# Kernel tuning notes

Measured on AMD Instinct MI355X. Metric: run time of the kernel, lower is better.

Reference implementation:

```python
import jax, jax.numpy as jnp
import numpy as np

N, K, D = 65536, 16, 64  # points, neighbors, d_out
EPS = 1e-5


def setup_inputs() -> dict:
    key = jax.random.key(0)
    ks = jax.random.split(key, 10)
    s = lambda fan: 1.0 / np.sqrt(fan)
    return {
        "p": jax.random.normal(ks[0], (N, K, 3), jnp.float32),
        "x": jax.random.normal(ks[1], (N, K, D), jnp.float32),
        # BiMLP: Conv1d(10, 2D, 1) -> BN -> ReLU -> Conv1d(2D, D, 1)
        "w1": jax.random.normal(ks[2], (10, 2 * D), jnp.float32) * s(10),
        "b1": jnp.zeros((2 * D,), jnp.float32),
        "g1": jnp.ones((2 * D,), jnp.float32),
        "be1": jnp.zeros((2 * D,), jnp.float32),
        "w2": jax.random.normal(ks[3], (2 * D, D), jnp.float32) * s(2 * D),
        "b2": jnp.zeros((D,), jnp.float32),
        # score_fn: Linear(2D, 2D, bias=False)
        "ws": jax.random.normal(ks[4], (2 * D, 2 * D), jnp.float32) * s(2 * D),
        # mlp_out: Linear(2D, D) -> BN -> ReLU
        "wo": jax.random.normal(ks[5], (2 * D, D), jnp.float32) * s(2 * D),
        "bo": jnp.zeros((D,), jnp.float32),
        "g2": jnp.ones((D,), jnp.float32),
        "be2": jnp.zeros((D,), jnp.float32),
    }


def reference(p, x, w1, b1, g1, be1, w2, b2, ws, wo, bo, g2, be2):
    # p: [N,K,3] neighbor coords (index 0 is the center), x: [N,K,D]
    center = p[:, :1, :]                                   # [N,1,3]
    diff = center - p                                      # [N,K,3]
    dist = jnp.sqrt(jnp.sum(diff * diff, axis=2, keepdims=True))  # [N,K,1]
    concat = jnp.concatenate(
        [jnp.broadcast_to(center, p.shape), p, diff, dist], axis=-1)  # [N,K,10]

    # 1x1 conv == per-point linear over channel dim
    h = jnp.einsum('nkc,cd->nkd', concat, w1) + b1          # [N,K,2D]
    # BatchNorm1d over (N,K) per channel (training-mode batch stats)
    mu = jnp.mean(h, axis=(0, 1))
    var = jnp.var(h, axis=(0, 1))
    h = (h - mu) * jax.lax.rsqrt(var + EPS) * g1 + be1
    h = jax.nn.relu(h)
    p_c = jnp.einsum('nkd,de->nke', h, w2) + b2             # [N,K,D]

    p_x = jnp.concatenate([p_c, x], axis=-1)                # [N,K,2D]
    # attention scores: linear (no bias) then softmax over neighbor dim (-2)
    scores = jax.nn.softmax(jnp.einsum('nkd,de->nke', p_x, ws), axis=-2)
    feat = jnp.sum(scores * p_x, axis=1)                    # [N,2D]

    out = feat @ wo + bo                                    # [N,D]
    mu2 = jnp.mean(out, axis=0)
    var2 = jnp.var(out, axis=0)
    out = (out - mu2) * jax.lax.rsqrt(var2 + EPS) * g2 + be2
    return jax.nn.relu(out)
```

## Files before the change

### kernel.cpp

```cpp
#include <hip/hip_runtime.h>
#include <math.h>

#define NPTS 65536
#define EPSV 1e-5f
#define B1G  256
#define B3G  1024

#define OFF_PART 0
#define OFF_S1   131072
#define OFF_S2   (OFF_S1+256)
#define OFF_PRE  (OFF_S2+128)

typedef unsigned int u32;
typedef short v8s __attribute__((ext_vector_type(8)));
typedef float v4f __attribute__((ext_vector_type(4)));

union F8 { v8s v; u32 u[4]; unsigned short s[8]; };

__device__ __forceinline__ u32 f2bf(float f){
  u32 u = __float_as_uint(f);
  return (u + 0x7fffu + ((u>>16)&1u)) >> 16;
}
__device__ __forceinline__ float bf2f(unsigned short s){ return __uint_as_float(((u32)s)<<16); }
__device__ __forceinline__ u32 packbf(float a, float b){
#if __has_builtin(__builtin_amdgcn_cvt_pk_bf16_f32)
  auto rv = __builtin_amdgcn_cvt_pk_bf16_f32(a, b);
  u32 u; __builtin_memcpy(&u, &rv, 4);
  return u;
#else
  return f2bf(a) | (f2bf(b)<<16);
#endif
}

__global__ __launch_bounds__(256) void k1_stats(const float* __restrict__ p, float* __restrict__ part1){
  int tid = blockIdx.x*256 + threadIdx.x;
  float M[55]; float s[10];
  #pragma unroll
  for(int i=0;i<55;i++) M[i]=0.f;
  #pragma unroll
  for(int i=0;i<10;i++) s[i]=0.f;
  for(int it=0; it<16; ++it){
    int r = it*65536 + tid;
    int n = r >> 4;
    int kk = r & 15;
    const float* pn = p + (size_t)n*48;
    float cx=pn[0], cy=pn[1], cz=pn[2];
    float ax=pn[kk*3+0], ay=pn[kk*3+1], az=pn[kk*3+2];
    float dx=cx-ax, dy=cy-ay, dz=cz-az;
    float dd = sqrtf(dx*dx+dy*dy+dz*dz);
    float c[10]={cx,cy,cz,ax,ay,az,dx,dy,dz,dd};
    #pragma unroll
    for(int i=0;i<10;i++) s[i]+=c[i];
    int idx=0;
    #pragma unroll
    for(int i=0;i<10;i++){
      #pragma unroll
      for(int j=i;j<10;j++){
        M[idx] = fmaf(c[i],c[j],M[idx]);
        idx++;
      }
    }
  }
  #pragma unroll
  for(int i=0;i<10;i++){
    for(int off=32; off>0; off>>=1) s[i] += __shfl_down(s[i], off, 64);
  }
  #pragma unroll
  for(int i=0;i<55;i++){
    for(int off=32; off>0; off>>=1) M[i] += __shfl_down(M[i], off, 64);
  }
  __shared__ float sm[4][65];
  int lane = threadIdx.x & 63, w = threadIdx.x >> 6;
  if(lane==0){
    #pragma unroll
    for(int i=0;i<10;i++) sm[w][i]=s[i];
    #pragma unroll
    for(int i=0;i<55;i++) sm[w][10+i]=M[i];
  }
  __syncthreads();
  if(threadIdx.x<65){
    float v = sm[0][threadIdx.x]+sm[1][threadIdx.x]+sm[2][threadIdx.x]+sm[3][threadIdx.x];
    part1[blockIdx.x*65 + threadIdx.x] = v;
  }
}

__device__ __forceinline__ int tri_idx(int i,int j){
  int a = i<j? i : j;
  int b = i<j? j : i;
  return 10*a - (a*(a-1))/2 + (b-a);
}
__global__ void k2_fin(const float* __restrict__ part1, const float* __restrict__ w1,
                       const float* __restrict__ g1, const float* __restrict__ be1,
                       float* __restrict__ stats1){
  __shared__ float S[65];
  int t = threadIdx.x;
  if(t<65){
    float a=0.f;
    for(int b=0;b<B1G;b++) a += part1[b*65+t];
    S[t]=a;
  }
  __syncthreads();
  float wc[10];
  #pragma unroll
  for(int c=0;c<10;c++) wc[c]=w1[c*128+t];
  float md=0.f;
  #pragma unroll
  for(int c=0;c<10;c++) md += S[c]*wc[c];
  const float invR = 1.0f/(float)(NPTS*16);
  md *= invR;
  float q=0.f;
  #pragma unroll
  for(int i=0;i<10;i++){
    float ti=0.f;
    #pragma unroll
    for(int j=0;j<10;j++) ti += S[10+tri_idx(i,j)]*wc[j];
    q = fmaf(ti, wc[i], q);
  }
  q *= invR;
  float var = q - md*md;
  float sc = g1[t]*rsqrtf(var+EPSV);
  float sh = be1[t] - md*sc;
  stats1[t]=sc;
  stats1[128+t]=sh;
}

__global__ __launch_bounds__(256,4) void k3_main(
    const float* __restrict__ p, const float* __restrict__ x,
    const float* __restrict__ w2, const float* __restrict__ b2,
    const float* __restrict__ wsm, const float* __restrict__ wo,
    const float* __restrict__ w1, const float* __restrict__ stats1,
    float* __restrict__ pre, float* __restrict__ part2)
{
  __shared__ __align__(16) unsigned short s_h [2][16][136];
  __shared__ __align__(16) unsigned short s_px[2][16][136];
  __shared__ __align__(16) float          s_lg[2][16][132];
  __shared__ __align__(16) unsigned short s_ft[16][136];

  const int tid  = threadIdx.x;
  const int w    = tid>>6;
  const int lane = tid&63;
  const int q    = lane>>4;
  const int c    = lane&15;

  v8s Bw1[2], Bw2[4], Bws[2][4], Bwo[4];
  #pragma unroll
  for(int t=0;t<2;t++){
    F8 f;
    #pragma unroll
    for(int j=0;j<8;j++){
      int k = q*8+j;
      f.s[j] = (unsigned short)(k<10 ? f2bf(w1[k*128 + 32*w + 16*t + c]) : 0);
    }
    Bw1[t]=f.v;
  }
  #pragma unroll
  for(int kk=0;kk<4;kk++){
    F8 f;
    #pragma unroll
    for(int j=0;j<8;j++){
      int pos = kk*32 + q*8 + j;
      int ch  = 32*(pos>>5) + 16*(pos&1) + ((pos>>1)&15);
      f.s[j]=(unsigned short)f2bf(w2[ch*64 + 16*w + c]);
    }
    Bw2[kk]=f.v;
  }
  #pragma unroll
  for(int t=0;t<2;t++){
    #pragma unroll
    for(int kk=0;kk<4;kk++){
      F8 f;
      #pragma unroll
      for(int j=0;j<8;j++) f.s[j]=(unsigned short)f2bf(wsm[(kk*32+q*8+j)*128 + 32*w + 16*t + c]);
      Bws[t][kk]=f.v;
    }
  }
  #pragma unroll
  for(int kk=0;kk<4;kk++){
    F8 f;
    #pragma unroll
    for(int j=0;j<8;j++) f.s[j]=(unsigned short)f2bf(wo[(kk*32+q*8+j)*64 + 16*w + c]);
    Bwo[kk]=f.v;
  }
  const float sc1a = stats1[32*w+c],    sh1a = stats1[128+32*w+c];
  const float sc1b = stats1[32*w+16+c], sh1b = stats1[128+32*w+16+c];
  const float b2v  = b2[16*w+c];

  const int n0s4 = w>>1;
  const int ch4  = 64*(w&1) + lane;
  const int lpos = 32*(ch4>>5) + 2*(ch4&15) + ((ch4>>4)&1);

  float a_s=0.f, a_q=0.f;
  const int base0 = blockIdx.x*64;

  for(int r=0;r<32;++r){
    const int base = base0 + 2*r;

    const float4* xg = (const float4*)(x + (size_t)base*1024);
    #pragma unroll
    for(int rr=0;rr<2;rr++){
      int f = tid + 256*rr;
      float4 v = xg[f];
      int n0 = f>>8, rem = f&255, pt = rem>>4, d4 = rem&15;
      *(uint2*)&s_px[n0][pt][64+4*d4] = make_uint2(packbf(v.x,v.y), packbf(v.z,v.w));
    }

    #pragma unroll
    for(int n0=0;n0<2;n0++){
      F8 fa;
      fa.u[0]=0u; fa.u[1]=0u; fa.u[2]=0u; fa.u[3]=0u;
      if(q<2){
        const float* pn = p + (size_t)(base+n0)*48;
        float cx=pn[0], cy=pn[1], cz=pn[2];
        float ax=pn[3*c], ay=pn[3*c+1], az=pn[3*c+2];
        float dx=cx-ax, dy=cy-ay, dz=cz-az;
        float dd=sqrtf(dx*dx+dy*dy+dz*dz);
        if(q==0){
          fa.u[0]=packbf(cx,cy); fa.u[1]=packbf(cz,ax);
          fa.u[2]=packbf(ay,az); fa.u[3]=packbf(dx,dy);
        }else{
          fa.u[0]=packbf(dz,dd);
        }
      }
      v4f z={0.f,0.f,0.f,0.f};
      v4f d0 = __builtin_amdgcn_mfma_f32_16x16x32_bf16(fa.v, Bw1[0], z, 0,0,0);
      v4f d1 = __builtin_amdgcn_mfma_f32_16x16x32_bf16(fa.v, Bw1[1], z, 0,0,0);
      #pragma unroll
      for(int i=0;i<4;i++){
        float v0 = fmaxf(0.f, fmaf(d0[i], sc1a, sh1a));
        float v1 = fmaxf(0.f, fmaf(d1[i], sc1b, sh1b));
        *(u32*)&s_h[n0][4*q+i][32*w+2*c] = packbf(v0,v1);
      }
    }
    __syncthreads();

    #pragma unroll
    for(int n0=0;n0<2;n0++){
      const v8s* Ar = (const v8s*)&s_h[n0][c][0];
      v4f acc={0.f,0.f,0.f,0.f};
      #pragma unroll
      for(int kk=0;kk<4;kk++)
        acc = __builtin_amdgcn_mfma_f32_16x16x32_bf16(Ar[kk*4+q], Bw2[kk], acc, 0,0,0);
      u32 pa = packbf(acc[0]+b2v, acc[1]+b2v);
      u32 pb = packbf(acc[2]+b2v, acc[3]+b2v);
      s_px[n0][4*q+0][16*w+c] = (unsigned short)pa;
      s_px[n0][4*q+1][16*w+c] = (unsigned short)(pa>>16);
      s_px[n0][4*q+2][16*w+c] = (unsigned short)pb;
      s_px[n0][4*q+3][16*w+c] = (unsigned short)(pb>>16);
    }
    __syncthreads();

    #pragma unroll
    for(int n0=0;n0<2;n0++){
      const v8s* Ar = (const v8s*)&s_px[n0][c][0];
      v4f l0={0.f,0.f,0.f,0.f}, l1={0.f,0.f,0.f,0.f};
      #pragma unroll
      for(int kk=0;kk<4;kk++){
        v8s a = Ar[kk*4+q];
        l0 = __builtin_amdgcn_mfma_f32_16x16x32_bf16(a, Bws[0][kk], l0, 0,0,0);
        l1 = __builtin_amdgcn_mfma_f32_16x16x32_bf16(a, Bws[1][kk], l1, 0,0,0);
      }
      #pragma unroll
      for(int i=0;i<4;i++)
        *(float2*)&s_lg[n0][4*q+i][32*w+2*c] = make_float2(l0[i], l1[i]);
    }
    __syncthreads();

    {
      float se=0.f, fe=0.f;
      #pragma unroll
      for(int pt=0;pt<16;pt++){
        float e = __expf(s_lg[n0s4][pt][lpos]);
        se += e;
        fe = fmaf(e, bf2f(s_px[n0s4][pt][ch4]), fe);
      }
      s_ft[(r&7)*2+n0s4][ch4] = (unsigned short)f2bf(__fdividef(fe,se));
    }
    __syncthreads();

    if((r&7)==7){
      const v8s* Ar = (const v8s*)&s_ft[c][0];
      v4f o={0.f,0.f,0.f,0.f};
      #pragma unroll
      for(int kk=0;kk<4;kk++)
        o = __builtin_amdgcn_mfma_f32_16x16x32_bf16(Ar[kk*4+q], Bwo[kk], o, 0,0,0);
      const int nb16 = base0 + (r>>3)*16;
      #pragma unroll
      for(int i=0;i<4;i++){
        float val = o[i];
        pre[(size_t)(nb16 + 4*q + i)*64 + 16*w + c] = val;
        a_s += val;
        a_q = fmaf(val,val,a_q);
      }
    }
  }

  a_s += __shfl_xor(a_s, 16, 64); a_s += __shfl_xor(a_s, 32, 64);
  a_q += __shfl_xor(a_q, 16, 64); a_q += __shfl_xor(a_q, 32, 64);
  if(q==0){
    part2[blockIdx.x*128 + 16*w + c]      = a_s;
    part2[blockIdx.x*128 + 64 + 16*w + c] = a_q;
  }
}

__global__ void k4_fin(const float* __restrict__ part2, const float* __restrict__ g2,
                       const float* __restrict__ be2, float* __restrict__ stats2){
  __shared__ float red[256];
  int t = threadIdx.x;
  int j = t & 127, g = t >> 7;
  float s = 0.f;
  for(int b=g;b<B3G;b+=2) s += part2[b*128 + j];
  red[t] = s;
  __syncthreads();
  if(t<64){
    float su = red[t]    + red[128+t];
    float qq = red[64+t] + red[192+t];
    float mu  = su/(float)NPTS;
    float var = qq/(float)NPTS - mu*mu;
    float sc = g2[t]*rsqrtf(var+EPSV);
    stats2[t]=sc;
    stats2[64+t]=be2[t]-mu*sc;
  }
}

__global__ __launch_bounds__(256) void k5_apply(const float* __restrict__ pre,
                                                const float* __restrict__ stats2,
                                                float* __restrict__ out){
  int i = blockIdx.x*256 + threadIdx.x;
  float4 v = ((const float4*)pre)[i];
  int d4 = i & 15;
  float4 sc = ((const float4*)stats2)[d4];
  float4 sh = ((const float4*)(stats2+64))[d4];
  float4 o;
  o.x = fmaxf(0.f, fmaf(v.x,sc.x,sh.x));
  o.y = fmaxf(0.f, fmaf(v.y,sc.y,sh.y));
  o.z = fmaxf(0.f, fmaf(v.z,sc.z,sh.z));
  o.w = fmaxf(0.f, fmaf(v.w,sc.w,sh.w));
  ((float4*)out)[i] = o;
}

extern "C" void kernel_launch(void* const* d_in, const int* in_sizes, int n_in,
                              void* d_out, int out_size, void* d_ws, size_t ws_size,
                              hipStream_t stream){
  (void)in_sizes; (void)n_in; (void)out_size; (void)ws_size;
  const float* p   = (const float*)d_in[0];
  const float* x   = (const float*)d_in[1];
  const float* w1  = (const float*)d_in[2];
  const float* g1  = (const float*)d_in[4];
  const float* be1 = (const float*)d_in[5];
  const float* w2  = (const float*)d_in[6];
  const float* b2  = (const float*)d_in[7];
  const float* wsm = (const float*)d_in[8];
  const float* wo  = (const float*)d_in[9];
  const float* g2  = (const float*)d_in[11];
  const float* be2 = (const float*)d_in[12];

  float* wsf    = (float*)d_ws;
  float* part1  = wsf + OFF_PART;
  float* part2  = wsf + OFF_PART;
  float* stats1 = wsf + OFF_S1;
  float* stats2 = wsf + OFF_S2;
  float* pre    = wsf + OFF_PRE;
  float* out    = (float*)d_out;

  k1_stats<<<B1G,256,0,stream>>>(p, part1);
  k2_fin  <<<1,128,0,stream>>>(part1, w1, g1, be1, stats1);
  k3_main <<<B3G,256,0,stream>>>(p,x,w2,b2,wsm,wo,w1,stats1,pre,part2);
  k4_fin  <<<1,256,0,stream>>>(part2,g2,be2,stats2);
  k5_apply<<<4096,256,0,stream>>>(pre,stats2,out);
}
```

Measured before the change: 620.6 us.

## Fuse softmax into MFMA epilogue, drop logit LDS buffer, double grid

Computes exp, the softmax sum and the weighted feature sum straight from the MFMA accumulator registers, reducing across neighbor rows with cross-lane shuffles. This removes the s_lg shared buffer and one barrier per iteration. The wo weight rows are permuted to match the new interleaved feature layout. The grid doubles to 2048 blocks, each handling half as many points, with launch bounds raised to 6 blocks per SM. The pre-activation buffer is written into the output and normalized in place, and k4 now reduces the larger partial array with 1024 threads.

```diff
diff --git a/kernel.cpp b/kernel.cpp
--- a/kernel.cpp
+++ b/kernel.cpp
@@ -4,12 +4,11 @@
 #define NPTS 65536
 #define EPSV 1e-5f
 #define B1G  256
-#define B3G  1024
+#define B3G  2048
 
 #define OFF_PART 0
-#define OFF_S1   131072
+#define OFF_S1   262144
 #define OFF_S2   (OFF_S1+256)
-#define OFF_PRE  (OFF_S2+128)
 
 typedef unsigned int u32;
 typedef short v8s __attribute__((ext_vector_type(8)));
@@ -124,7 +123,7 @@
   stats1[128+t]=sh;
 }
 
-__global__ __launch_bounds__(256,4) void k3_main(
+__global__ __launch_bounds__(256,6) void k3_main(
     const float* __restrict__ p, const float* __restrict__ x,
     const float* __restrict__ w2, const float* __restrict__ b2,
     const float* __restrict__ wsm, const float* __restrict__ wo,
@@ -133,7 +132,6 @@
 {
   __shared__ __align__(16) unsigned short s_h [2][16][136];
   __shared__ __align__(16) unsigned short s_px[2][16][136];
-  __shared__ __align__(16) float          s_lg[2][16][132];
   __shared__ __align__(16) unsigned short s_ft[16][136];
 
   const int tid  = threadIdx.x;
@@ -178,21 +176,21 @@
   for(int kk=0;kk<4;kk++){
     F8 f;
     #pragma unroll
-    for(int j=0;j<8;j++) f.s[j]=(unsigned short)f2bf(wo[(kk*32+q*8+j)*64 + 16*w + c]);
+    for(int j=0;j<8;j++){
+      int pos = kk*32 + q*8 + j;
+      int ch  = 32*(pos>>5) + 16*(pos&1) + ((pos>>1)&15);
+      f.s[j]=(unsigned short)f2bf(wo[ch*64 + 16*w + c]);
+    }
     Bwo[kk]=f.v;
   }
   const float sc1a = stats1[32*w+c],    sh1a = stats1[128+32*w+c];
   const float sc1b = stats1[32*w+16+c], sh1b = stats1[128+32*w+16+c];
   const float b2v  = b2[16*w+c];
 
-  const int n0s4 = w>>1;
-  const int ch4  = 64*(w&1) + lane;
-  const int lpos = 32*(ch4>>5) + 2*(ch4&15) + ((ch4>>4)&1);
-
   float a_s=0.f, a_q=0.f;
-  const int base0 = blockIdx.x*64;
-
-  for(int r=0;r<32;++r){
+  const int base0 = blockIdx.x*32;
+
+  for(int r=0;r<16;++r){
     const int base = base0 + 2*r;
 
     const float4* xg = (const float4*)(x + (size_t)base*1024);
@@ -259,21 +257,24 @@
         l0 = __builtin_amdgcn_mfma_f32_16x16x32_bf16(a, Bws[0][kk], l0, 0,0,0);
         l1 = __builtin_amdgcn_mfma_f32_16x16x32_bf16(a, Bws[1][kk], l1, 0,0,0);
       }
-      #pragma unroll
-      for(int i=0;i<4;i++)
-        *(float2*)&s_lg[n0][4*q+i][32*w+2*c] = make_float2(l0[i], l1[i]);
-    }
-    __syncthreads();
-
-    {
-      float se=0.f, fe=0.f;
-      #pragma unroll
-      for(int pt=0;pt<16;pt++){
-        float e = __expf(s_lg[n0s4][pt][lpos]);
-        se += e;
-        fe = fmaf(e, bf2f(s_px[n0s4][pt][ch4]), fe);
-      }
-      s_ft[(r&7)*2+n0s4][ch4] = (unsigned short)f2bf(__fdividef(fe,se));
+      float se0=0.f, fe0=0.f, se1=0.f, fe1=0.f;
+      #pragma unroll
+      for(int i=0;i<4;i++){
+        float p0 = bf2f(s_px[n0][4*q+i][32*w+c]);
+        float p1 = bf2f(s_px[n0][4*q+i][32*w+16+c]);
+        float e0 = __expf(l0[i]);
+        float e1 = __expf(l1[i]);
+        se0 += e0; fe0 = fmaf(e0,p0,fe0);
+        se1 += e1; fe1 = fmaf(e1,p1,fe1);
+      }
+      se0 += __shfl_xor(se0,16,64); se0 += __shfl_xor(se0,32,64);
+      fe0 += __shfl_xor(fe0,16,64); fe0 += __shfl_xor(fe0,32,64);
+      se1 += __shfl_xor(se1,16,64); se1 += __shfl_xor(se1,32,64);
+      fe1 += __shfl_xor(fe1,16,64); fe1 += __shfl_xor(fe1,32,64);
+      if(q==0){
+        *(u32*)&s_ft[(r&7)*2+n0][32*w+2*c] =
+          packbf(__fdividef(fe0,se0), __fdividef(fe1,se1));
+      }
     }
     __syncthreads();
 
@@ -304,16 +305,17 @@
 
 __global__ void k4_fin(const float* __restrict__ part2, const float* __restrict__ g2,
                        const float* __restrict__ be2, float* __restrict__ stats2){
-  __shared__ float red[256];
+  __shared__ float red[1024];
   int t = threadIdx.x;
   int j = t & 127, g = t >> 7;
   float s = 0.f;
-  for(int b=g;b<B3G;b+=2) s += part2[b*128 + j];
+  for(int b=g;b<B3G;b+=8) s += part2[b*128 + j];
   red[t] = s;
   __syncthreads();
   if(t<64){
-    float su = red[t]    + red[128+t];
-    float qq = red[64+t] + red[192+t];
+    float su=0.f, qq=0.f;
+    #pragma unroll
+    for(int gg=0;gg<8;gg++){ su += red[gg*128+t]; qq += red[gg*128+64+t]; }
     float mu  = su/(float)NPTS;
     float var = qq/(float)NPTS - mu*mu;
     float sc = g2[t]*rsqrtf(var+EPSV);
@@ -359,12 +361,11 @@
   float* part2  = wsf + OFF_PART;
   float* stats1 = wsf + OFF_S1;
   float* stats2 = wsf + OFF_S2;
-  float* pre    = wsf + OFF_PRE;
   float* out    = (float*)d_out;
 
   k1_stats<<<B1G,256,0,stream>>>(p, part1);
   k2_fin  <<<1,128,0,stream>>>(part1, w1, g1, be1, stats1);
-  k3_main <<<B3G,256,0,stream>>>(p,x,w2,b2,wsm,wo,w1,stats1,pre,part2);
-  k4_fin  <<<1,256,0,stream>>>(part2,g2,be2,stats2);
-  k5_apply<<<4096,256,0,stream>>>(pre,stats2,out);
-}
+  k3_main <<<B3G,256,0,stream>>>(p,x,w2,b2,wsm,wo,w1,stats1,out,part2);
+  k4_fin  <<<1,1024,0,stream>>>(part2,g2,be2,stats2);
+  k5_apply<<<4096,256,0,stream>>>(out,stats2,out);
+}
```

New measurement: 806.3 us. +29.9%, slower.
